# Kernel tuning notes

Measured on AMD Instinct MI355X. Metric: run time of the kernel, lower is better.

Reference implementation:

```python
import jax, jax.numpy as jnp
import numpy as np

NUM_EXPERTS = 8
TOP_K = 2
D_HIDDEN = 2048
D_EXPERT = 1024
N_TOKENS = 4096


def setup_inputs() -> dict:
    key = jax.random.key(0)
    ks = jax.random.split(key, 8)
    s_d = 1.0 / np.sqrt(D_HIDDEN).astype(np.float32)
    s_h = 1.0 / np.sqrt(D_EXPERT).astype(np.float32)
    return {
        "x": jax.random.normal(ks[0], (N_TOKENS, D_HIDDEN), jnp.float32),
        "W_g": jax.random.normal(ks[1], (D_HIDDEN, NUM_EXPERTS), jnp.float32) * s_d,
        "W_gate": jax.random.normal(ks[2], (NUM_EXPERTS, D_HIDDEN, D_EXPERT), jnp.float32) * s_d,
        "W_up": jax.random.normal(ks[3], (NUM_EXPERTS, D_HIDDEN, D_EXPERT), jnp.float32) * s_d,
        "W_down": jax.random.normal(ks[4], (NUM_EXPERTS, D_EXPERT, D_HIDDEN), jnp.float32) * s_h,
        "Ws_gate": jax.random.normal(ks[5], (D_HIDDEN, D_EXPERT), jnp.float32) * s_d,
        "Ws_up": jax.random.normal(ks[6], (D_HIDDEN, D_EXPERT), jnp.float32) * s_d,
        "Ws_down": jax.random.normal(ks[7], (D_EXPERT, D_HIDDEN), jnp.float32) * s_h,
    }


def reference(x, W_g, W_gate, W_up, W_down, Ws_gate, Ws_up, Ws_down):
    # Router: softmax logits -> top-k scores/indices (fused_gating_topk)
    probs = jax.nn.softmax(x @ W_g, axis=-1)                      # [N, E]
    scores, idx = jax.lax.top_k(probs, TOP_K)                     # [N, K]
    # Per-(token, expert) combine weight; zero for unrouted experts.
    combine = (jax.nn.one_hot(idx, NUM_EXPERTS, dtype=x.dtype) * scores[..., None]).sum(axis=1)  # [N, E]

    # Routed experts: fused gate/up SiLU with per-token weight scaling, then down-proj.
    gate = jnp.einsum('nd,edh->enh', x, W_gate)                   # [E, N, H]
    up = jnp.einsum('nd,edh->enh', x, W_up)                       # [E, N, H]
    h = jax.nn.silu(gate) * up * combine.T[:, :, None]            # weight=0 kills unrouted tokens
    out = jnp.einsum('enh,ehd->nd', h, W_down)                    # [N, D]

    # Shared expert applied to every token (no routing weight).
    shared = (jax.nn.silu(x @ Ws_gate) * (x @ Ws_up)) @ Ws_down
    return out + shared
```

## Files before the change

### kernel.cpp

```cpp
#include <hip/hip_runtime.h>
#include <cstdint>
#include <cstddef>

#define N_TOK 4096
#define D_HID 2048
#define D_EXP 1024
#define NE 8
#define N_ROUTED (N_TOK * 2)
#define N_ROWS (N_ROUTED + N_TOK)
#define MAX_BLK 112

typedef unsigned short u16;
typedef __bf16 bf16x8 __attribute__((ext_vector_type(8)));
typedef float f32x4 __attribute__((ext_vector_type(4)));

constexpr size_t OFF_XB    = 0;
constexpr size_t OFF_WG    = OFF_XB    + 16777216;
constexpr size_t OFF_WU    = OFF_WG    + 33554432;
constexpr size_t OFF_WD    = OFF_WU    + 33554432;
constexpr size_t OFF_WSG   = OFF_WD    + 33554432;
constexpr size_t OFF_WSU   = OFF_WSG   + 4194304;
constexpr size_t OFF_WSD   = OFF_WSU   + 4194304;
constexpr size_t OFF_H     = OFF_WSD   + 4194304;
constexpr size_t OFF_ROWS  = OFF_H     + 25165824;
constexpr size_t OFF_WSLOT = OFF_ROWS  + 49152;
constexpr size_t OFF_SEG   = OFF_WSLOT + 49152;
constexpr size_t OFF_BLK   = OFF_SEG   + 128;
constexpr size_t OFF_TOPI  = OFF_BLK   + 768;
constexpr size_t OFF_TOPW  = OFF_TOPI  + 32768;
constexpr size_t OFF_INV   = OFF_TOPW  + 32768;
constexpr size_t OFF_H2    = OFF_WG;

__device__ __forceinline__ u16 f32_to_bf16(float f) {
    union { float f; unsigned int u; } c; c.f = f;
    unsigned int u = c.u;
    return (u16)((u + 0x7FFFu + ((u >> 16) & 1u)) >> 16);
}
__device__ __forceinline__ float bf16_to_f32(u16 v) {
    union { unsigned int u; float f; } c; c.u = ((unsigned int)v) << 16;
    return c.f;
}

__device__ __forceinline__ void gld_lds16(const u16* g, u16* l) {
    __builtin_amdgcn_global_load_lds(
        (const __attribute__((address_space(1))) void*)g,
        (__attribute__((address_space(3))) void*)l,
        16, 0, 0);
}

__global__ void cvt_x_kernel(const float* __restrict__ x, u16* __restrict__ xb) {
    size_t i = ((size_t)blockIdx.x * 256 + threadIdx.x) * 8;
    float4 a = *(const float4*)(x + i);
    float4 b = *(const float4*)(x + i + 4);
    union { u16 us[8]; uint4 v; } r;
    r.us[0] = f32_to_bf16(a.x); r.us[1] = f32_to_bf16(a.y);
    r.us[2] = f32_to_bf16(a.z); r.us[3] = f32_to_bf16(a.w);
    r.us[4] = f32_to_bf16(b.x); r.us[5] = f32_to_bf16(b.y);
    r.us[6] = f32_to_bf16(b.z); r.us[7] = f32_to_bf16(b.w);
    *(uint4*)(xb + i) = r.v;
}

__global__ void prep_gu_kernel(const float* __restrict__ Wg, const float* __restrict__ Wu,
                               const float* __restrict__ Wsg, const float* __restrict__ Wsu,
                               u16* __restrict__ Wg_t, u16* __restrict__ Wu_t,
                               u16* __restrict__ Wsg_t, u16* __restrict__ Wsu_t) {
    __shared__ float tile[64][66];
    const int z = blockIdx.z;
    const float* src; u16* dst;
    if (z < 8)        { src = Wg + (size_t)z * (D_HID * D_EXP);       dst = Wg_t + (size_t)z * (D_HID * D_EXP); }
    else if (z < 16)  { src = Wu + (size_t)(z - 8) * (D_HID * D_EXP); dst = Wu_t + (size_t)(z - 8) * (D_HID * D_EXP); }
    else if (z == 16) { src = Wsg; dst = Wsg_t; }
    else              { src = Wsu; dst = Wsu_t; }
    const int c0 = blockIdx.x * 64, r0 = blockIdx.y * 64;
    const int tid = threadIdx.x;
    const int tx = tid & 15, ty = tid >> 4;
#pragma unroll
    for (int i = 0; i < 4; i++) {
        float4 v = *(const float4*)(src + (size_t)(r0 + ty + 16 * i) * D_EXP + c0 + tx * 4);
        tile[ty + 16 * i][tx * 4 + 0] = v.x;
        tile[ty + 16 * i][tx * 4 + 1] = v.y;
        tile[ty + 16 * i][tx * 4 + 2] = v.z;
        tile[ty + 16 * i][tx * 4 + 3] = v.w;
    }
    __syncthreads();
    const int kx = tid & 7, cy = tid >> 3;
#pragma unroll
    for (int j = 0; j < 2; j++) {
        int n = cy + 32 * j;
        union { u16 us[8]; uint4 v; } r;
#pragma unroll
        for (int m = 0; m < 8; m++) r.us[m] = f32_to_bf16(tile[kx * 8 + m][n]);
        *(uint4*)(dst + (size_t)(c0 + n) * D_HID + r0 + kx * 8) = r.v;
    }
}

__global__ void prep_d_kernel(const float* __restrict__ Wd, const float* __restrict__ Wsd,
                              u16* __restrict__ Wd_t, u16* __restrict__ Wsd_t) {
    __shared__ float tile[64][66];
    const int z = blockIdx.z;
    const float* src; u16* dst;
    if (z < 8) { src = Wd + (size_t)z * (D_EXP * D_HID); dst = Wd_t + (size_t)z * (D_EXP * D_HID); }
    else       { src = Wsd; dst = Wsd_t; }
    const int c0 = blockIdx.x * 64, r0 = blockIdx.y * 64;
    const int tid = threadIdx.x;
    const int tx = tid & 15, ty = tid >> 4;
#pragma unroll
    for (int i = 0; i < 4; i++) {
        float4 v = *(const float4*)(src + (size_t)(r0 + ty + 16 * i) * D_HID + c0 + tx * 4);
        tile[ty + 16 * i][tx * 4 + 0] = v.x;
        tile[ty + 16 * i][tx * 4 + 1] = v.y;
        tile[ty + 16 * i][tx * 4 + 2] = v.z;
        tile[ty + 16 * i][tx * 4 + 3] = v.w;
    }
    __syncthreads();
    const int kx = tid & 7, cy = tid >> 3;
#pragma unroll
    for (int j = 0; j < 2; j++) {
        int n = cy + 32 * j;
        union { u16 us[8]; uint4 v; } r;
#pragma unroll
        for (int m = 0; m < 8; m++) r.us[m] = f32_to_bf16(tile[kx * 8 + m][n]);
        *(uint4*)(dst + (size_t)(c0 + n) * D_EXP + r0 + kx * 8) = r.v;
    }
}

__global__ void router_kernel(const float* __restrict__ x, const float* __restrict__ Wg,
                              int* __restrict__ topi, float* __restrict__ topw) {
    const int wave = threadIdx.x >> 6, lane = threadIdx.x & 63;
    const int t = blockIdx.x * 4 + wave;
    const float* xr = x + (size_t)t * D_HID;
    float acc[8] = {0.f, 0.f, 0.f, 0.f, 0.f, 0.f, 0.f, 0.f};
    for (int k = lane; k < D_HID; k += 64) {
        float xv = xr[k];
        float4 w0 = *(const float4*)(Wg + k * 8);
        float4 w1 = *(const float4*)(Wg + k * 8 + 4);
        acc[0] += xv * w0.x; acc[1] += xv * w0.y; acc[2] += xv * w0.z; acc[3] += xv * w0.w;
        acc[4] += xv * w1.x; acc[5] += xv * w1.y; acc[6] += xv * w1.z; acc[7] += xv * w1.w;
    }
#pragma unroll
    for (int e = 0; e < 8; e++)
#pragma unroll
        for (int off = 32; off > 0; off >>= 1)
            acc[e] += __shfl_xor(acc[e], off);
    if (lane == 0) {
        float mx = acc[0];
#pragma unroll
        for (int e = 1; e < 8; e++) mx = fmaxf(mx, acc[e]);
        float p[8], sum = 0.f;
#pragma unroll
        for (int e = 0; e < 8; e++) { p[e] = __expf(acc[e] - mx); sum += p[e]; }
        int i0 = 0; float b0 = p[0];
#pragma unroll
        for (int e = 1; e < 8; e++) if (p[e] > b0) { b0 = p[e]; i0 = e; }
        int i1 = -1; float b1 = -1.f;
#pragma unroll
        for (int e = 0; e < 8; e++) if (e != i0 && p[e] > b1) { b1 = p[e]; i1 = e; }
        float inv = 1.f / sum;
        topi[t * 2] = i0;  topi[t * 2 + 1] = i1;
        topw[t * 2] = b0 * inv; topw[t * 2 + 1] = b1 * inv;
    }
}

__global__ void builder_kernel(const int* __restrict__ topi, const float* __restrict__ topw,
                               int* __restrict__ rows, float* __restrict__ wslot,
                               int* __restrict__ seg, int* __restrict__ blkmap,
                               int* __restrict__ inv) {
    __shared__ int cnt[8], offs[8];
    const int tid = threadIdx.x;
    if (tid < 8) cnt[tid] = 0;
    __syncthreads();
    for (int i = tid; i < N_TOK * 2; i += 256) atomicAdd(&cnt[topi[i]], 1);
    __syncthreads();
    if (tid == 0) {
        int run = 0;
        for (int e = 0; e < 8; e++) {
            offs[e] = run; seg[e] = run; seg[16 + e] = cnt[e]; run += cnt[e];
        }
        seg[8] = N_ROUTED; seg[16 + 8] = N_TOK;
        int nb = 0;
        for (int e = 0; e < 9; e++) {
            int L = (e < 8) ? cnt[e] : N_TOK;
            for (int rb = 0; rb * 128 < L; rb++) blkmap[nb++] = (e << 8) | rb;
        }
        seg[10] = nb;
    }
    __syncthreads();
    for (int i = tid; i < N_TOK * 2; i += 256) {
        int e = topi[i];
        int p = atomicAdd(&offs[e], 1);
        rows[p] = i >> 1;
        wslot[p] = topw[i];
        inv[i] = p;
    }
    for (int t = tid; t < N_TOK; t += 256) {
        rows[N_ROUTED + t] = t;
        wslot[N_ROUTED + t] = 1.0f;
    }
}

__global__ __launch_bounds__(256, 2)
void gemm1_kernel(const u16* __restrict__ xb,
                  const u16* __restrict__ Wg_t, const u16* __restrict__ Wu_t,
                  const u16* __restrict__ Wsg_t, const u16* __restrict__ Wsu_t,
                  const int* __restrict__ rows, const float* __restrict__ wslot,
                  const int* __restrict__ seg, const int* __restrict__ blkmap,
                  u16* __restrict__ h) {
    if ((int)blockIdx.x >= seg[10]) return;
    const int code = blkmap[blockIdx.x];
    const int e = code >> 8, rb = code & 255;
    const int s = seg[e], L = seg[e + 16];
    const u16* Bg = (e < NE) ? Wg_t + (size_t)e * D_EXP * D_HID : Wsg_t;
    const u16* Bu = (e < NE) ? Wu_t + (size_t)e * D_EXP * D_HID : Wsu_t;
    const int cbase = blockIdx.y * 128;

    __shared__ u16 As[128 * 32];
    __shared__ u16 Bgs[128 * 32];
    __shared__ u16 Bus[128 * 32];
    __shared__ int tok_s[128];

    const int tid = threadIdx.x;
    if (tid < 128) {
        int lr = rb * 128 + tid;
        tok_s[tid] = rows[s + (lr < L ? lr : 0)];
    }
    __syncthreads();

    const int lane = tid & 63, wave = tid >> 6;
    const int wm = wave & 1, wn = wave >> 1;
    const int ln = lane & 15, quad = lane >> 4;

    const int lr16 = lane >> 2;
    const int c8 = (lane & 3) * 8;
    const int ra0 = wave * 32 + lr16, ra1 = ra0 + 16;
    const size_t ta0 = (size_t)tok_s[ra0] * D_HID + c8;
    const size_t ta1 = (size_t)tok_s[ra1] * D_HID + c8;
    const u16* pbg0 = Bg + (size_t)(cbase + ra0) * D_HID + c8;
    const u16* pbg1 = Bg + (size_t)(cbase + ra1) * D_HID + c8;
    const u16* pbu0 = Bu + (size_t)(cbase + ra0) * D_HID + c8;
    const u16* pbu1 = Bu + (size_t)(cbase + ra1) * D_HID + c8;
    u16* lA0 = As + (size_t)(wave * 32) * 32;
    u16* lA1 = As + (size_t)(wave * 32 + 16) * 32;
    u16* lG0 = Bgs + (size_t)(wave * 32) * 32;
    u16* lG1 = Bgs + (size_t)(wave * 32 + 16) * 32;
    u16* lU0 = Bus + (size_t)(wave * 32) * 32;
    u16* lU1 = Bus + (size_t)(wave * 32 + 16) * 32;

    f32x4 accg[4][4], accu[4][4];
    const f32x4 zero = {0.f, 0.f, 0.f, 0.f};
#pragma unroll
    for (int i = 0; i < 4; i++)
#pragma unroll
        for (int j = 0; j < 4; j++) { accg[i][j] = zero; accu[i][j] = zero; }

    for (int k0 = 0; k0 < D_HID; k0 += 32) {
        __syncthreads();
        gld_lds16(xb + ta0 + k0, lA0);
        gld_lds16(xb + ta1 + k0, lA1);
        gld_lds16(pbg0 + k0, lG0);
        gld_lds16(pbg1 + k0, lG1);
        gld_lds16(pbu0 + k0, lU0);
        gld_lds16(pbu1 + k0, lU1);
        __syncthreads();
        bf16x8 af[4];
#pragma unroll
        for (int sm = 0; sm < 4; sm++)
            af[sm] = *(const bf16x8*)&As[(wm * 64 + sm * 16 + ln) * 32 + quad * 8];
#pragma unroll
        for (int sn = 0; sn < 4; sn++) {
            const bf16x8 bgf = *(const bf16x8*)&Bgs[(wn * 64 + sn * 16 + ln) * 32 + quad * 8];
            const bf16x8 buf = *(const bf16x8*)&Bus[(wn * 64 + sn * 16 + ln) * 32 + quad * 8];
#pragma unroll
            for (int sm = 0; sm < 4; sm++) {
                accg[sm][sn] = __builtin_amdgcn_mfma_f32_16x16x32_bf16(af[sm], bgf, accg[sm][sn], 0, 0, 0);
                accu[sm][sn] = __builtin_amdgcn_mfma_f32_16x16x32_bf16(af[sm], buf, accu[sm][sn], 0, 0, 0);
            }
        }
    }
#pragma unroll
    for (int sm = 0; sm < 4; sm++) {
#pragma unroll
        for (int r = 0; r < 4; r++) {
            int lrow = rb * 128 + wm * 64 + sm * 16 + quad * 4 + r;
            if (lrow >= L) continue;
            int pos = s + lrow;
            float w = wslot[pos];
#pragma unroll
            for (int sn = 0; sn < 4; sn++) {
                float g = accg[sm][sn][r];
                float u = accu[sm][sn][r];
                float hv = (g / (1.f + __expf(-g))) * u * w;
                int col = cbase + wn * 64 + sn * 16 + ln;
                h[(size_t)pos * D_EXP + col] = f32_to_bf16(hv);
            }
        }
    }
}

__global__ __launch_bounds__(256, 2)
void gemm2_kernel(const u16* __restrict__ h,
                  const u16* __restrict__ Wd_t, const u16* __restrict__ Wsd_t,
                  const int* __restrict__ seg, const int* __restrict__ blkmap,
                  u16* __restrict__ h2) {
    if ((int)blockIdx.x >= seg[10]) return;
    const int code = blkmap[blockIdx.x];
    const int e = code >> 8, rb = code & 255;
    const int s = seg[e], L = seg[e + 16];
    const u16* B = (e < NE) ? Wd_t + (size_t)e * D_HID * D_EXP : Wsd_t;
    const int cbase = blockIdx.y * 128;

    __shared__ u16 As[128 * 32];
    __shared__ u16 Bs[128 * 32];

    const int tid = threadIdx.x;
    const int lane = tid & 63, wave = tid >> 6;
    const int wm = wave & 1, wn = wave >> 1;
    const int ln = lane & 15, quad = lane >> 4;

    const int lr16 = lane >> 2;
    const int c8 = (lane & 3) * 8;
    const int ra0 = wave * 32 + lr16, ra1 = ra0 + 16;
    const u16* pa0 = h + (size_t)(s + rb * 128 + ra0) * D_EXP + c8;
    const u16* pa1 = h + (size_t)(s + rb * 128 + ra1) * D_EXP + c8;
    const u16* pb0 = B + (size_t)(cbase + ra0) * D_EXP + c8;
    const u16* pb1 = B + (size_t)(cbase + ra1) * D_EXP + c8;
    u16* lA0 = As + (size_t)(wave * 32) * 32;
    u16* lA1 = As + (size_t)(wave * 32 + 16) * 32;
    u16* lB0 = Bs + (size_t)(wave * 32) * 32;
    u16* lB1 = Bs + (size_t)(wave * 32 + 16) * 32;

    f32x4 acc[4][4];
    const f32x4 zero = {0.f, 0.f, 0.f, 0.f};
#pragma unroll
    for (int i = 0; i < 4; i++)
#pragma unroll
        for (int j = 0; j < 4; j++) acc[i][j] = zero;

    for (int k0 = 0; k0 < D_EXP; k0 += 32) {
        __syncthreads();
        gld_lds16(pa0 + k0, lA0);
        gld_lds16(pa1 + k0, lA1);
        gld_lds16(pb0 + k0, lB0);
        gld_lds16(pb1 + k0, lB1);
        __syncthreads();
        bf16x8 af[4];
#pragma unroll
        for (int sm = 0; sm < 4; sm++)
            af[sm] = *(const bf16x8*)&As[(wm * 64 + sm * 16 + ln) * 32 + quad * 8];
#pragma unroll
        for (int sn = 0; sn < 4; sn++) {
            const bf16x8 bfg = *(const bf16x8*)&Bs[(wn * 64 + sn * 16 + ln) * 32 + quad * 8];
#pragma unroll
            for (int sm = 0; sm < 4; sm++)
                acc[sm][sn] = __builtin_amdgcn_mfma_f32_16x16x32_bf16(af[sm], bfg, acc[sm][sn], 0, 0, 0);
        }
    }
#pragma unroll
    for (int sm = 0; sm < 4; sm++) {
#pragma unroll
        for (int r = 0; r < 4; r++) {
            int lrow = rb * 128 + wm * 64 + sm * 16 + quad * 4 + r;
            if (lrow >= L) continue;
            size_t slot = (size_t)(s + lrow);
#pragma unroll
            for (int sn = 0; sn < 4; sn++) {
                int col = cbase + wn * 64 + sn * 16 + ln;
                h2[slot * D_HID + col] = f32_to_bf16(acc[sm][sn][r]);
            }
        }
    }
}

__global__ void combine_kernel(const u16* __restrict__ h2, const int* __restrict__ inv,
                               float* __restrict__ out) {
    const int t = blockIdx.x;
    const int d = threadIdx.x * 8;
    const size_t r0 = (size_t)inv[t * 2] * D_HID + d;
    const size_t r1 = (size_t)inv[t * 2 + 1] * D_HID + d;
    const size_t r2 = (size_t)(N_ROUTED + t) * D_HID + d;
    union { uint4 v; u16 us[8]; } a, b, c;
    a.v = *(const uint4*)(h2 + r0);
    b.v = *(const uint4*)(h2 + r1);
    c.v = *(const uint4*)(h2 + r2);
    float4 lo, hi;
    lo.x = bf16_to_f32(a.us[0]) + bf16_to_f32(b.us[0]) + bf16_to_f32(c.us[0]);
    lo.y = bf16_to_f32(a.us[1]) + bf16_to_f32(b.us[1]) + bf16_to_f32(c.us[1]);
    lo.z = bf16_to_f32(a.us[2]) + bf16_to_f32(b.us[2]) + bf16_to_f32(c.us[2]);
    lo.w = bf16_to_f32(a.us[3]) + bf16_to_f32(b.us[3]) + bf16_to_f32(c.us[3]);
    hi.x = bf16_to_f32(a.us[4]) + bf16_to_f32(b.us[4]) + bf16_to_f32(c.us[4]);
    hi.y = bf16_to_f32(a.us[5]) + bf16_to_f32(b.us[5]) + bf16_to_f32(c.us[5]);
    hi.z = bf16_to_f32(a.us[6]) + bf16_to_f32(b.us[6]) + bf16_to_f32(c.us[6]);
    hi.w = bf16_to_f32(a.us[7]) + bf16_to_f32(b.us[7]) + bf16_to_f32(c.us[7]);
    float* o = out + (size_t)t * D_HID + d;
    *(float4*)o = lo;
    *(float4*)(o + 4) = hi;
}

extern "C" void kernel_launch(void* const* d_in, const int* in_sizes, int n_in,
                              void* d_out, int out_size, void* d_ws, size_t ws_size,
                              hipStream_t stream) {
    const float* x       = (const float*)d_in[0];
    const float* W_g     = (const float*)d_in[1];
    const float* W_gate  = (const float*)d_in[2];
    const float* W_up    = (const float*)d_in[3];
    const float* W_down  = (const float*)d_in[4];
    const float* Ws_gate = (const float*)d_in[5];
    const float* Ws_up   = (const float*)d_in[6];
    const float* Ws_down = (const float*)d_in[7];
    float* out = (float*)d_out;
    char* ws = (char*)d_ws;

    u16*   xb    = (u16*)(ws + OFF_XB);
    u16*   Wg_t  = (u16*)(ws + OFF_WG);
    u16*   Wu_t  = (u16*)(ws + OFF_WU);
    u16*   Wd_t  = (u16*)(ws + OFF_WD);
    u16*   Wsg_t = (u16*)(ws + OFF_WSG);
    u16*   Wsu_t = (u16*)(ws + OFF_WSU);
    u16*   Wsd_t = (u16*)(ws + OFF_WSD);
    u16*   h     = (u16*)(ws + OFF_H);
    u16*   h2    = (u16*)(ws + OFF_H2);
    int*   rows  = (int*)(ws + OFF_ROWS);
    float* wslot = (float*)(ws + OFF_WSLOT);
    int*   seg   = (int*)(ws + OFF_SEG);
    int*   blkmap= (int*)(ws + OFF_BLK);
    int*   topi  = (int*)(ws + OFF_TOPI);
    float* topw  = (float*)(ws + OFF_TOPW);
    int*   inv   = (int*)(ws + OFF_INV);

    cvt_x_kernel<<<dim3((N_TOK * D_HID) / (256 * 8)), dim3(256), 0, stream>>>(x, xb);
    prep_gu_kernel<<<dim3(D_EXP / 64, D_HID / 64, 18), dim3(256), 0, stream>>>(
        W_gate, W_up, Ws_gate, Ws_up, Wg_t, Wu_t, Wsg_t, Wsu_t);
    prep_d_kernel<<<dim3(D_HID / 64, D_EXP / 64, 9), dim3(256), 0, stream>>>(
        W_down, Ws_down, Wd_t, Wsd_t);

    router_kernel<<<dim3(N_TOK / 4), dim3(256), 0, stream>>>(x, W_g, topi, topw);
    builder_kernel<<<dim3(1), dim3(256), 0, stream>>>(topi, topw, rows, wslot, seg, blkmap, inv);

    gemm1_kernel<<<dim3(MAX_BLK, D_EXP / 128), dim3(256), 0, stream>>>(
        xb, Wg_t, Wu_t, Wsg_t, Wsu_t, rows, wslot, seg, blkmap, h);
    gemm2_kernel<<<dim3(MAX_BLK, D_HID / 128), dim3(256), 0, stream>>>(
        h, Wd_t, Wsd_t, seg, blkmap, h2);
    combine_kernel<<<dim3(N_TOK), dim3(256), 0, stream>>>(h2, inv, out);
}
```

Measured before the change: 563.0 us.

## Double-buffer LDS tiles and XOR-swizzle LDS columns in both expert GEMMs

Both grouped GEMM kernels now keep two LDS buffers per operand. The next K-slice's async global-to-LDS loads are issued before computing on the current slice, which removes one barrier per iteration and overlaps memory latency with MFMA work. The 16-byte column chunks are also XOR-swizzled by row on the load side, with a matching permuted read index, to reduce LDS bank conflicts on the fragment reads. In exchange the LDS footprint doubles, to 48KB per block in gemm1, which could limit occupancy.

```diff
diff --git a/kernel.cpp b/kernel.cpp
--- a/kernel.cpp
+++ b/kernel.cpp
@@ -213,9 +213,9 @@
     const u16* Bu = (e < NE) ? Wu_t + (size_t)e * D_EXP * D_HID : Wsu_t;
     const int cbase = blockIdx.y * 128;
 
-    __shared__ u16 As[128 * 32];
-    __shared__ u16 Bgs[128 * 32];
-    __shared__ u16 Bus[128 * 32];
+    __shared__ u16 As[2][128 * 32];
+    __shared__ u16 Bgs[2][128 * 32];
+    __shared__ u16 Bus[2][128 * 32];
     __shared__ int tok_s[128];
 
     const int tid = threadIdx.x;
@@ -230,7 +230,8 @@
     const int ln = lane & 15, quad = lane >> 4;
 
     const int lr16 = lane >> 2;
-    const int c8 = (lane & 3) * 8;
+    const int swz = (lr16 >> 1) & 3;
+    const int c8 = (((lane & 3) ^ swz)) * 8;
     const int ra0 = wave * 32 + lr16, ra1 = ra0 + 16;
     const size_t ta0 = (size_t)tok_s[ra0] * D_HID + c8;
     const size_t ta1 = (size_t)tok_s[ra1] * D_HID + c8;
@@ -238,12 +239,7 @@
     const u16* pbg1 = Bg + (size_t)(cbase + ra1) * D_HID + c8;
     const u16* pbu0 = Bu + (size_t)(cbase + ra0) * D_HID + c8;
     const u16* pbu1 = Bu + (size_t)(cbase + ra1) * D_HID + c8;
-    u16* lA0 = As + (size_t)(wave * 32) * 32;
-    u16* lA1 = As + (size_t)(wave * 32 + 16) * 32;
-    u16* lG0 = Bgs + (size_t)(wave * 32) * 32;
-    u16* lG1 = Bgs + (size_t)(wave * 32 + 16) * 32;
-    u16* lU0 = Bus + (size_t)(wave * 32) * 32;
-    u16* lU1 = Bus + (size_t)(wave * 32 + 16) * 32;
+    const int l0 = (wave * 32) * 32, l1 = (wave * 32 + 16) * 32;
 
     f32x4 accg[4][4], accu[4][4];
     const f32x4 zero = {0.f, 0.f, 0.f, 0.f};
@@ -252,23 +248,35 @@
 #pragma unroll
         for (int j = 0; j < 4; j++) { accg[i][j] = zero; accu[i][j] = zero; }
 
+    const int q8 = (quad ^ ((ln >> 1) & 3)) * 8;
+
+    gld_lds16(xb + ta0, &As[0][l0]);
+    gld_lds16(xb + ta1, &As[0][l1]);
+    gld_lds16(pbg0, &Bgs[0][l0]);
+    gld_lds16(pbg1, &Bgs[0][l1]);
+    gld_lds16(pbu0, &Bus[0][l0]);
+    gld_lds16(pbu1, &Bus[0][l1]);
+
     for (int k0 = 0; k0 < D_HID; k0 += 32) {
+        const int cur = (k0 >> 5) & 1;
         __syncthreads();
-        gld_lds16(xb + ta0 + k0, lA0);
-        gld_lds16(xb + ta1 + k0, lA1);
-        gld_lds16(pbg0 + k0, lG0);
-        gld_lds16(pbg1 + k0, lG1);
-        gld_lds16(pbu0 + k0, lU0);
-        gld_lds16(pbu1 + k0, lU1);
-        __syncthreads();
+        if (k0 + 32 < D_HID) {
+            const int nxt = cur ^ 1;
+            gld_lds16(xb + ta0 + k0 + 32, &As[nxt][l0]);
+            gld_lds16(xb + ta1 + k0 + 32, &As[nxt][l1]);
+            gld_lds16(pbg0 + k0 + 32, &Bgs[nxt][l0]);
+            gld_lds16(pbg1 + k0 + 32, &Bgs[nxt][l1]);
+            gld_lds16(pbu0 + k0 + 32, &Bus[nxt][l0]);
+            gld_lds16(pbu1 + k0 + 32, &Bus[nxt][l1]);
+        }
         bf16x8 af[4];
 #pragma unroll
         for (int sm = 0; sm < 4; sm++)
-            af[sm] = *(const bf16x8*)&As[(wm * 64 + sm * 16 + ln) * 32 + quad * 8];
+            af[sm] = *(const bf16x8*)&As[cur][(wm * 64 + sm * 16 + ln) * 32 + q8];
 #pragma unroll
         for (int sn = 0; sn < 4; sn++) {
-            const bf16x8 bgf = *(const bf16x8*)&Bgs[(wn * 64 + sn * 16 + ln) * 32 + quad * 8];
-            const bf16x8 buf = *(const bf16x8*)&Bus[(wn * 64 + sn * 16 + ln) * 32 + quad * 8];
+            const bf16x8 bgf = *(const bf16x8*)&Bgs[cur][(wn * 64 + sn * 16 + ln) * 32 + q8];
+            const bf16x8 buf = *(const bf16x8*)&Bus[cur][(wn * 64 + sn * 16 + ln) * 32 + q8];
 #pragma unroll
             for (int sm = 0; sm < 4; sm++) {
                 accg[sm][sn] = __builtin_amdgcn_mfma_f32_16x16x32_bf16(af[sm], bgf, accg[sm][sn], 0, 0, 0);
@@ -308,8 +316,8 @@
     const u16* B = (e < NE) ? Wd_t + (size_t)e * D_HID * D_EXP : Wsd_t;
     const int cbase = blockIdx.y * 128;
 
-    __shared__ u16 As[128 * 32];
-    __shared__ u16 Bs[128 * 32];
+    __shared__ u16 As[2][128 * 32];
+    __shared__ u16 Bs[2][128 * 32];
 
     const int tid = threadIdx.x;
     const int lane = tid & 63, wave = tid >> 6;
@@ -317,16 +325,14 @@
     const int ln = lane & 15, quad = lane >> 4;
 
     const int lr16 = lane >> 2;
-    const int c8 = (lane & 3) * 8;
+    const int swz = (lr16 >> 1) & 3;
+    const int c8 = (((lane & 3) ^ swz)) * 8;
     const int ra0 = wave * 32 + lr16, ra1 = ra0 + 16;
     const u16* pa0 = h + (size_t)(s + rb * 128 + ra0) * D_EXP + c8;
     const u16* pa1 = h + (size_t)(s + rb * 128 + ra1) * D_EXP + c8;
     const u16* pb0 = B + (size_t)(cbase + ra0) * D_EXP + c8;
     const u16* pb1 = B + (size_t)(cbase + ra1) * D_EXP + c8;
-    u16* lA0 = As + (size_t)(wave * 32) * 32;
-    u16* lA1 = As + (size_t)(wave * 32 + 16) * 32;
-    u16* lB0 = Bs + (size_t)(wave * 32) * 32;
-    u16* lB1 = Bs + (size_t)(wave * 32 + 16) * 32;
+    const int l0 = (wave * 32) * 32, l1 = (wave * 32 + 16) * 32;
 
     f32x4 acc[4][4];
     const f32x4 zero = {0.f, 0.f, 0.f, 0.f};
@@ -335,20 +341,30 @@
 #pragma unroll
         for (int j = 0; j < 4; j++) acc[i][j] = zero;
 
+    const int q8 = (quad ^ ((ln >> 1) & 3)) * 8;
+
+    gld_lds16(pa0, &As[0][l0]);
+    gld_lds16(pa1, &As[0][l1]);
+    gld_lds16(pb0, &Bs[0][l0]);
+    gld_lds16(pb1, &Bs[0][l1]);
+
     for (int k0 = 0; k0 < D_EXP; k0 += 32) {
+        const int cur = (k0 >> 5) & 1;
         __syncthreads();
-        gld_lds16(pa0 + k0, lA0);
-        gld_lds16(pa1 + k0, lA1);
-        gld_lds16(pb0 + k0, lB0);
-        gld_lds16(pb1 + k0, lB1);
-        __syncthreads();
+        if (k0 + 32 < D_EXP) {
+            const int nxt = cur ^ 1;
+            gld_lds16(pa0 + k0 + 32, &As[nxt][l0]);
+            gld_lds16(pa1 + k0 + 32, &As[nxt][l1]);
+            gld_lds16(pb0 + k0 + 32, &Bs[nxt][l0]);
+            gld_lds16(pb1 + k0 + 32, &Bs[nxt][l1]);
+        }
         bf16x8 af[4];
 #pragma unroll
         for (int sm = 0; sm < 4; sm++)
-            af[sm] = *(const bf16x8*)&As[(wm * 64 + sm * 16 + ln) * 32 + quad * 8];
+            af[sm] = *(const bf16x8*)&As[cur][(wm * 64 + sm * 16 + ln) * 32 + q8];
 #pragma unroll
         for (int sn = 0; sn < 4; sn++) {
-            const bf16x8 bfg = *(const bf16x8*)&Bs[(wn * 64 + sn * 16 + ln) * 32 + quad * 8];
+            const bf16x8 bfg = *(const bf16x8*)&Bs[cur][(wn * 64 + sn * 16 + ln) * 32 + q8];
 #pragma unroll
             for (int sm = 0; sm < 4; sm++)
                 acc[sm][sn] = __builtin_amdgcn_mfma_f32_16x16x32_bf16(af[sm], bfg, acc[sm][sn], 0, 0, 0);
```

After: 566.6 us. No clear change (+0.6%).
